# Kernel tuning notes

Hardware: AMD Instinct MI355X
Metric: run time of the kernel (lower is better)

## Reference

```python
import jax, jax.numpy as jnp
import numpy as np

ENZ_DIM, CPD_DIM, OUT_DIM = 1280, 256, 512
B, L_ENZ, L_CPD = 32, 512, 128
SCALE = OUT_DIM ** 0.5


def _linear_params(key, d_in, d_out):
    k1, k2 = jax.random.split(key)
    lim = 1.0 / np.sqrt(d_in)
    W = jax.random.uniform(k1, (d_in, d_out), jnp.float32, -lim, lim)
    b = jax.random.uniform(k2, (d_out,), jnp.float32, -lim, lim)
    return W, b


def setup_inputs() -> dict:
    key = jax.random.key(0)
    ks = jax.random.split(key, 16)
    inp = {
        "enz_node_feature": jax.random.normal(ks[0], (B, L_ENZ, ENZ_DIM), jnp.float32),
        "substrate_node_feature": jax.random.normal(ks[1], (B, L_CPD, CPD_DIM), jnp.float32),
        "product_node_feature": jax.random.normal(ks[2], (B, L_CPD, CPD_DIM), jnp.float32),
        "enz_node_feature_mask": jnp.ones((B, L_ENZ), dtype=bool),
        "substrate_node_feature_mask": jnp.ones((B, L_CPD), dtype=bool),
        "product_node_feature_mask": jnp.ones((B, L_CPD), dtype=bool),
        "interaction_weight": jax.random.normal(ks[3], (B, L_CPD, L_ENZ), jnp.float32),
    }
    # cross_attn_enzyme: query=enz (ENZ_DIM), key/value=cpd (CPD_DIM)
    inp["enz_Wq"], inp["enz_bq"] = _linear_params(ks[4], ENZ_DIM, OUT_DIM)
    inp["enz_Wk"], inp["enz_bk"] = _linear_params(ks[5], CPD_DIM, OUT_DIM)
    inp["enz_Wv"], inp["enz_bv"] = _linear_params(ks[6], CPD_DIM, OUT_DIM)
    # cross_attn_substrate: query=cpd, key/value=enz
    inp["sub_Wq"], inp["sub_bq"] = _linear_params(ks[7], CPD_DIM, OUT_DIM)
    inp["sub_Wk"], inp["sub_bk"] = _linear_params(ks[8], ENZ_DIM, OUT_DIM)
    inp["sub_Wv"], inp["sub_bv"] = _linear_params(ks[9], ENZ_DIM, OUT_DIM)
    # cross_attn_product: query=cpd, key/value=enz
    inp["prod_Wq"], inp["prod_bq"] = _linear_params(ks[10], CPD_DIM, OUT_DIM)
    inp["prod_Wk"], inp["prod_bk"] = _linear_params(ks[11], ENZ_DIM, OUT_DIM)
    inp["prod_Wv"], inp["prod_bv"] = _linear_params(ks[12], ENZ_DIM, OUT_DIM)
    return inp


def _cross_attn(q_in, k_in, v_in, q_mask, k_mask, Wq, bq, Wk, bk, Wv, bv, attn_bias=None):
    q = q_in @ Wq + bq          # [B, Lq, D]
    k = k_in @ Wk + bk          # [B, Lk, D]
    v = v_in @ Wv + bv          # [B, Lk, D]
    scores = jnp.einsum("bqd,bkd->bqk", q, k) / SCALE
    if attn_bias is not None:
        scores = scores + attn_bias
    mask = q_mask[:, :, None] & k_mask[:, None, :]   # [B, Lq, Lk]
    scores = jnp.where(mask, scores, -1e9)
    w = jax.nn.softmax(scores, axis=-1)
    return jnp.einsum("bqk,bkd->bqd", w, v)


def reference(enz_node_feature, substrate_node_feature, product_node_feature,
              enz_node_feature_mask, substrate_node_feature_mask, product_node_feature_mask,
              interaction_weight,
              enz_Wq, enz_bq, enz_Wk, enz_bk, enz_Wv, enz_bv,
              sub_Wq, sub_bq, sub_Wk, sub_bk, sub_Wv, sub_bv,
              prod_Wq, prod_bq, prod_Wk, prod_bk, prod_Wv, prod_bv):
    subs_pocket_weight = interaction_weight                       # [B, L_cpd, L_enz]
    pocket_subs_weight = jnp.swapaxes(interaction_weight, 1, 2)   # [B, L_enz, L_cpd]

    enzyme_subs = _cross_attn(enz_node_feature, substrate_node_feature, substrate_node_feature,
                              enz_node_feature_mask, substrate_node_feature_mask,
                              enz_Wq, enz_bq, enz_Wk, enz_bk, enz_Wv, enz_bv,
                              attn_bias=pocket_subs_weight)
    subs_enzyme = _cross_attn(substrate_node_feature, enz_node_feature, enz_node_feature,
                              substrate_node_feature_mask, enz_node_feature_mask,
                              sub_Wq, sub_bq, sub_Wk, sub_bk, sub_Wv, sub_bv,
                              attn_bias=subs_pocket_weight)
    # product path reuses cross_attn_enzyme weights for enz->prod (as in torch code)
    enzyme_prod = _cross_attn(enz_node_feature, product_node_feature, product_node_feature,
                              enz_node_feature_mask, product_node_feature_mask,
                              enz_Wq, enz_bq, enz_Wk, enz_bk, enz_Wv, enz_bv)
    prod_enzyme = _cross_attn(product_node_feature, enz_node_feature, enz_node_feature,
                              product_node_feature_mask, enz_node_feature_mask,
                              prod_Wq, prod_bq, prod_Wk, prod_bk, prod_Wv, prod_bv)

    return jnp.concatenate([enzyme_subs.mean(axis=1), subs_enzyme.mean(axis=1),
                            enzyme_prod.mean(axis=1), prod_enzyme.mean(axis=1)], axis=-1)
```

## Files before the change

kernel.cpp:

```cpp
#include <hip/hip_runtime.h>
#include <cstdint>
#include <cstddef>


#define SCALE_INV 0.044194173824159216f

typedef short bf16x8 __attribute__((ext_vector_type(8)));
typedef float f32x4  __attribute__((ext_vector_type(4)));

__device__ __forceinline__ ushort f2bf(float f) {
  union { float f; unsigned u; } c; c.f = f;
  unsigned u = c.u + 0x7fffu + ((c.u >> 16) & 1u);
  return (ushort)(u >> 16);
}
__device__ __forceinline__ float bf2f(ushort h) {
  return __uint_as_float(((unsigned)h) << 16);
}
__device__ __forceinline__ void gload16(const ushort* g, ushort* l) {
  __builtin_amdgcn_global_load_lds(
      (const __attribute__((address_space(1))) void*)g,
      (__attribute__((address_space(3))) void*)l, 16, 0, 0);
}

__device__ __forceinline__ void cvt8(const float* __restrict__ in,
                                     ushort* __restrict__ out, int blk, int n) {
  int i = (blk * 256 + (int)threadIdx.x) * 8;
  if (i >= n) return;
  float4 a = *(const float4*)(in + i);
  float4 b = *(const float4*)(in + i + 4);
  ushort o[8] = { f2bf(a.x), f2bf(a.y), f2bf(a.z), f2bf(a.w),
                  f2bf(b.x), f2bf(b.y), f2bf(b.z), f2bf(b.w) };
  *(uint4*)(out + i) = *(uint4*)o;
}

__global__ __launch_bounds__(256) void prep_fused(
    const float* __restrict__ enz, const float* __restrict__ sub,
    const float* __restrict__ prod,
    ushort* __restrict__ enz_b, ushort* __restrict__ sub_b, ushort* __restrict__ prod_b,
    const float* __restrict__ enz_Wq, const float* __restrict__ enz_Wk,
    const float* __restrict__ sub_Wq, const float* __restrict__ sub_Wk,
    const float* __restrict__ prod_Wq, const float* __restrict__ prod_Wk,
    ushort* __restrict__ eWq_b, ushort* __restrict__ eWk_b,
    ushort* __restrict__ sWq_b, ushort* __restrict__ sWk_b,
    ushort* __restrict__ pWq_b, ushort* __restrict__ pWk_b,
    const float* __restrict__ enz_bq, const float* __restrict__ sub_bq,
    const float* __restrict__ prod_bq,
    const float* __restrict__ enz_bv, const float* __restrict__ sub_bv,
    const float* __restrict__ prod_bv,
    float* __restrict__ u_s_s, float* __restrict__ u_p_s,
    float* __restrict__ u_e_s,
    float* __restrict__ zero_base, float* __restrict__ out)
{
  const int f = blockIdx.x, t = threadIdx.x;
  if (f < 10240) { cvt8(enz, enz_b, f, 20971520); return; }
  if (f < 10752) { cvt8(sub, sub_b, f - 10240, 1048576); return; }
  if (f < 11264) { cvt8(prod, prod_b, f - 10752, 1048576); return; }
  if (f < 12416) {
    const int l = f - 11264;
    if (l < 320)       cvt8(enz_Wq,  eWq_b, l,        655360);
    else if (l < 640)  cvt8(sub_Wk,  sWk_b, l - 320,  655360);
    else if (l < 960)  cvt8(prod_Wk, pWk_b, l - 640,  655360);
    else if (l < 1024) cvt8(enz_Wk,  eWk_b, l - 960,  131072);
    else if (l < 1088) cvt8(sub_Wq,  sWq_b, l - 1024, 131072);
    else               cvt8(prod_Wq, pWq_b, l - 1088, 131072);
    return;
  }
  if (f < 12592) {
    const int g = f - 12416;
    const float* W; const float* bv; float* U; int d0;
    if (g < 80)       { W = sub_Wk;  bv = sub_bq;  U = u_s_s; d0 = g * 16; }
    else if (g < 160) { W = prod_Wk; bv = prod_bq; U = u_p_s; d0 = (g - 80) * 16; }
    else              { W = enz_Wk;  bv = enz_bq;  U = u_e_s; d0 = (g - 160) * 16; }
    const int r = t >> 4, i = t & 15, d = d0 + r;
    const float* row = W + (size_t)d * 512;
    float s = 0.f;
#pragma unroll
    for (int j = 0; j < 32; j++) s += row[i + j * 16] * bv[i + j * 16];
    s += __shfl_xor(s, 1); s += __shfl_xor(s, 2);
    s += __shfl_xor(s, 4); s += __shfl_xor(s, 8);
    if (i == 0) U[d] = s * SCALE_INV;
    return;
  }
  if (f < 13168) { zero_base[(f - 12592) * 256 + t] = 0.f; return; }
  {
    const int idx = (f - 13168) * 256 + t;
    const int col = idx & 2047;
    const int q = col >> 9, n = col & 511;
    const float* bvp = (q == 1) ? sub_bv : (q == 3) ? prod_bv : enz_bv;
    out[idx] = bvp[n];
  }
}

__device__ __forceinline__ void mfma_tile(
    const ushort* __restrict__ A, int lda,
    const ushort* __restrict__ Bt, int ldb, int K,
    int bm, int bn, ushort* AsBase, ushort* BsBase, f32x4 (&acc)[4][4])
{
  const int t = threadIdx.x, wave = t >> 6, lane = t & 63;
  const int srow = wave * 16 + (lane >> 2);
  const int sseg = (lane & 3) * 8;
  const ushort* Ag0 = A + (size_t)(bm + srow) * lda + sseg;
  const ushort* Ag1 = Ag0 + (size_t)64 * lda;
  const ushort* Bg0 = Bt + (size_t)(bn + srow) * ldb + sseg;
  const ushort* Bg1 = Bg0 + (size_t)64 * ldb;
  ushort* AsP0 = AsBase + srow * 32 + sseg;
  ushort* AsP1 = AsP0 + 64 * 32;
  ushort* BsP0 = BsBase + srow * 32 + sseg;
  ushort* BsP1 = BsP0 + 64 * 32;
  const int wm = (wave >> 1) * 64, wn = (wave & 1) * 64;
  const int fl = lane & 15, fq = lane >> 4;
  const bf16x8* ArP = (const bf16x8*)(AsBase + (wm + fl) * 32 + fq * 8);
  const bf16x8* BrP = (const bf16x8*)(BsBase + (wn + fl) * 32 + fq * 8);
  for (int k0 = 0; k0 < K; k0 += 32) {
    __syncthreads();
    gload16(Ag0 + k0, AsP0);
    gload16(Ag1 + k0, AsP1);
    gload16(Bg0 + k0, BsP0);
    gload16(Bg1 + k0, BsP1);
    __syncthreads();
    bf16x8 af[4], bfr[4];
#pragma unroll
    for (int i = 0; i < 4; i++) af[i] = ArP[i * 64];
#pragma unroll
    for (int j = 0; j < 4; j++) bfr[j] = BrP[j * 64];
#pragma unroll
    for (int i = 0; i < 4; i++)
#pragma unroll
      for (int j = 0; j < 4; j++)
        acc[i][j] = __builtin_amdgcn_mfma_f32_16x16x32_bf16(af[i], bfr[j], acc[i][j], 0, 0, 0);
  }
}

__global__ __launch_bounds__(256) void fold_w3(
    const ushort* __restrict__ eWq_b, const ushort* __restrict__ eWk_b,
    const ushort* __restrict__ sWq_b, const ushort* __restrict__ sWk_b,
    const ushort* __restrict__ pWq_b, const ushort* __restrict__ pWk_b,
    const ushort* __restrict__ sub_b, const ushort* __restrict__ prod_b,
    const ushort* __restrict__ enz_b,
    const float* __restrict__ u_e_s, const float* __restrict__ u_s_s,
    const float* __restrict__ u_p_s,
    ushort* __restrict__ W3t, float* __restrict__ t_es, float* __restrict__ t_ep,
    float* __restrict__ t_se, float* __restrict__ t_pe)
{
  __shared__ __align__(16) ushort As[128 * 32];
  __shared__ __align__(16) ushort Bs[128 * 32];
  __shared__ float us[256];
  __shared__ float us2[2][1280];
  const int f = blockIdx.x, t = threadIdx.x;
  if (f >= 76) {
    const int g2 = f - 76;
    for (int i = t; i < 1280; i += 256) { us2[0][i] = u_s_s[i]; us2[1][i] = u_p_s[i]; }
    __syncthreads();
    const int row = g2 * 64 + (t >> 2), lane4 = t & 3;
    const ushort* xr = enz_b + (size_t)row * 1280;
    float ss = 0.f, sp = 0.f;
#pragma unroll
    for (int q = 0; q < 40; ++q) {
      const int c0 = q * 32 + lane4 * 8;
      bf16x8 v = *(const bf16x8*)(xr + c0);
#pragma unroll
      for (int i = 0; i < 8; ++i) {
        const float x = bf2f((ushort)v[i]);
        ss += x * us2[0][c0 + i];
        sp += x * us2[1][c0 + i];
      }
    }
    ss += __shfl_xor(ss, 1); ss += __shfl_xor(ss, 2);
    sp += __shfl_xor(sp, 1); sp += __shfl_xor(sp, 2);
    if (lane4 == 0) { t_se[row] = ss; t_pe[row] = sp; }
    return;
  }
  if (f >= 60) {
    const int g = f - 60, path = g >> 3, blk8 = g & 7;
    const ushort* Xb = path ? prod_b : sub_b;
    float* T = path ? t_ep : t_es;
    us[t] = u_e_s[t];
    __syncthreads();
#pragma unroll
    for (int e = 0; e < 2; ++e) {
      const int row = blk8 * 512 + e * 256 + t;
      const ushort* xr = Xb + (size_t)row * 256;
      float s = 0.f;
      for (int c = 0; c < 256; c += 8) {
        bf16x8 v = *(const bf16x8*)(xr + c);
#pragma unroll
        for (int i = 0; i < 8; ++i) s += bf2f((ushort)v[i]) * us[c + i];
      }
      T[row] = s;
    }
    return;
  }
  const int seg = f / 20, l = f % 20;
  const int bm = (l / 10) * 128, bn = (l % 10) * 128;
  const ushort* A  = (seg == 0) ? eWk_b : (seg == 1) ? sWq_b : pWq_b;
  const ushort* Bt = (seg == 0) ? eWq_b : (seg == 1) ? sWk_b : pWk_b;
  f32x4 acc[4][4] = {};
  mfma_tile(A, 512, Bt, 512, 512, bm, bn, As, Bs, acc);
  const int lane = t & 63, wave = t >> 6;
  const int wm = (wave >> 1) * 64, wn = (wave & 1) * 64;
  const int fl = lane & 15, fq = lane >> 4;
#pragma unroll
  for (int i = 0; i < 4; i++)
#pragma unroll
    for (int j = 0; j < 4; j++) {
      const int col = bn + wn + j * 16 + fl;
#pragma unroll
      for (int r = 0; r < 4; r++) {
        const int row = seg * 256 + bm + wm + i * 16 + fq * 4 + r;
        W3t[(size_t)row * 1280 + col] = f2bf(acc[i][j][r]);
      }
    }
}

__device__ __forceinline__ void yg_stage_unit(
    const ushort* __restrict__ gbase, int k0, int u,
    ushort* ldsTile, int wv, int l, int srow8, int scol)
{
  const int row0 = u * 64 + wv * 8 + srow8;
  gload16(gbase + (size_t)row0 * 1280 + k0 + scol,
          ldsTile + u * 4096 + wv * 512 + l * 8);
}

__device__ __forceinline__ bf16x8 yg_frag(const ushort* tile, int row, int kk, int fq) {
  const int X = (kk * 64 + fq * 16) ^ ((row & 7) << 4);
  return *(const bf16x8*)((const char*)tile + row * 128 + X);
}

__global__ __launch_bounds__(512, 4) void y_gemm(
    const ushort* __restrict__ A,
    const ushort* __restrict__ B,
    ushort* __restrict__ Y)
{
  extern __shared__ __align__(16) ushort lds[];
  const int t = threadIdx.x;
  const int wv = t >> 6, l = t & 63;
  const int fl = l & 15, fq = l >> 4;
  const int f = blockIdx.x;
  const int xcd = f & 7, slot = f >> 3;
  const int mt = xcd * 16 + (slot >> 2), nt = slot & 3;
  const int bm = mt * 128, bn = nt * 192;
  const int wm = (wv >> 2) * 64, wn = (wv & 3) * 48;
  const int srow8 = l >> 3;
  const int scol = 8 * ((l & 7) ^ srow8);
  const ushort* Ag = A + (size_t)bm * 1280;
  const ushort* Bg = B + (size_t)bn * 1280;

  ushort* A0 = lds;
  ushort* B0 = lds + 8192;
  ushort* A1 = lds + 20480;
  ushort* B1 = lds + 28672;

  f32x4 acc[4][3] = {};

#pragma unroll
  for (int u = 0; u < 2; ++u) yg_stage_unit(Ag, 0, u, A0, wv, l, srow8, scol);
#pragma unroll
  for (int u = 0; u < 3; ++u) yg_stage_unit(Bg, 0, u, B0, wv, l, srow8, scol);
#pragma unroll
  for (int u = 0; u < 2; ++u) yg_stage_unit(Ag, 64, u, A1, wv, l, srow8, scol);
  asm volatile("s_waitcnt vmcnt(2)" ::: "memory");
  __builtin_amdgcn_s_barrier();
  __builtin_amdgcn_sched_barrier(0);

  for (int j = 0; j < 20; ++j) {
    const int p = j & 1;
    const ushort* At = p ? A1 : A0;
    const ushort* Bt = p ? B1 : B0;
    ushort* Bo = p ? B0 : B1;
    const int kn = (j + 1) * 64;

    bf16x8 bf_[3][2];
#pragma unroll
    for (int n = 0; n < 3; ++n)
#pragma unroll
      for (int kk = 0; kk < 2; ++kk)
        bf_[n][kk] = yg_frag(Bt, wn + n * 16 + fl, kk, fq);

#pragma unroll
    for (int mp = 0; mp < 4; ++mp) {
      if (mp < 3 && j < 19) yg_stage_unit(Bg, kn, mp, Bo, wv, l, srow8, scol);
      bf16x8 a0[2];
#pragma unroll
      for (int kk = 0; kk < 2; ++kk)
        a0[kk] = yg_frag(At, wm + mp * 16 + fl, kk, fq);
      __builtin_amdgcn_s_setprio(1);
#pragma unroll
      for (int kk = 0; kk < 2; ++kk)
#pragma unroll
        for (int n = 0; n < 3; ++n)
          acc[mp][n] = __builtin_amdgcn_mfma_f32_16x16x32_bf16(
              a0[kk], bf_[n][kk], acc[mp][n], 0, 0, 0);
      __builtin_amdgcn_s_setprio(0);
    }

    asm volatile("" ::: "memory");
    __builtin_amdgcn_s_barrier();
    if (j + 2 < 20) {
      ushort* Ao = (ushort*)At;
#pragma unroll
      for (int u = 0; u < 2; ++u)
        yg_stage_unit(Ag, (j + 2) * 64, u, Ao, wv, l, srow8, scol);
    }
    if (j < 18) asm volatile("s_waitcnt vmcnt(2)" ::: "memory");
    else        asm volatile("s_waitcnt vmcnt(0)" ::: "memory");
    __builtin_amdgcn_s_barrier();
    __builtin_amdgcn_sched_barrier(0);
  }

#pragma unroll
  for (int m = 0; m < 4; ++m)
#pragma unroll
    for (int n = 0; n < 3; ++n)
#pragma unroll
      for (int r = 0; r < 4; ++r) {
        const int row = bm + wm + m * 16 + fq * 4 + r;
        const int col = bn + wn + n * 16 + fl;
        Y[(size_t)row * 768 + col] = f2bf(acc[m][n][r]);
      }
}

__global__ __launch_bounds__(256) void score_fused(
    const ushort* __restrict__ Y, const ushort* __restrict__ sub_b,
    const ushort* __restrict__ prod_b, const float* __restrict__ iw,
    const float* __restrict__ t_es, const float* __restrict__ t_ep,
    const float* __restrict__ t_se, const float* __restrict__ t_pe,
    float* __restrict__ Sc_se, float* __restrict__ Sc_pe,
    float* __restrict__ l_se, float* __restrict__ l_pe,
    float* __restrict__ wsum_es, float* __restrict__ wsum_ep)
{
  __shared__ __align__(16) ushort As[128 * 32];
  __shared__ __align__(16) ushort Bs[128 * 32];
  __shared__ float red[2][128];
  __shared__ float red2[2][128];
  const int f = blockIdx.x, t = threadIdx.x;
  const int lane = t & 63, wave = t >> 6;
  const int wm = (wave >> 1) * 64, wn = (wave & 1) * 64;
  const int fl = lane & 15, fq = lane >> 4;
  f32x4 acc[4][4] = {};

  if (f < 256) {
    const int path = f >> 7, l = f & 127, b = l & 31, mt = l >> 5;
    const int bm = mt * 128;
    const ushort* X = (path ? prod_b : sub_b) + (size_t)b * 32768;
    mfma_tile(Y + (size_t)b * 512 * 768, 768, X, 256, 256, bm, 0, As, Bs, acc);
    const size_t ib = (size_t)b * 65536;
    const float* Tp = (path ? t_ep : t_es) + b * 128;
    float tvv[4];
#pragma unroll
    for (int j = 0; j < 4; j++) tvv[j] = Tp[wn + j * 16 + fl];
    float rsum[4][4];
#pragma unroll
    for (int i = 0; i < 4; i++)
#pragma unroll
      for (int r = 0; r < 4; r++) rsum[i][r] = 0.f;
#pragma unroll
    for (int i = 0; i < 4; i++)
#pragma unroll
      for (int j = 0; j < 4; j++)
#pragma unroll
        for (int r = 0; r < 4; r++) {
          const int row = wm + i * 16 + fq * 4 + r;
          const int col = wn + j * 16 + fl;
          float s = acc[i][j][r] * SCALE_INV + tvv[j];
          if (path == 0) s += iw[ib + (size_t)col * 512 + (bm + row)];
          const float e = __expf(s);
          acc[i][j][r] = e;
          rsum[i][r] += e;
        }
#pragma unroll
    for (int m = 1; m <= 8; m <<= 1)
#pragma unroll
      for (int i = 0; i < 4; i++)
#pragma unroll
        for (int r = 0; r < 4; r++)
          rsum[i][r] += __shfl_xor(rsum[i][r], m);
    if (fl == 0)
#pragma unroll
      for (int i = 0; i < 4; i++)
#pragma unroll
        for (int r = 0; r < 4; r++)
          red[wave & 1][wm + i * 16 + fq * 4 + r] = rsum[i][r];
    __syncthreads();
    float csum[4] = { 0.f, 0.f, 0.f, 0.f };
#pragma unroll
    for (int i = 0; i < 4; i++)
#pragma unroll
      for (int r = 0; r < 4; r++) {
        const int row = wm + i * 16 + fq * 4 + r;
        const float invr = 1.f / (red[0][row] + red[1][row]);
#pragma unroll
        for (int j = 0; j < 4; j++) csum[j] += acc[i][j][r] * invr;
      }
#pragma unroll
    for (int m = 16; m <= 32; m <<= 1)
#pragma unroll
      for (int j = 0; j < 4; j++) csum[j] += __shfl_xor(csum[j], m);
    if (fq == 0)
#pragma unroll
      for (int j = 0; j < 4; j++) red2[wave >> 1][wn + j * 16 + fl] = csum[j];
    __syncthreads();
    float* ws = (path ? wsum_ep : wsum_es) + b * 128;
    if (t < 128) atomicAdd(&ws[t], red2[0][t] + red2[1][t]);
  } else {
    const int g = f - 256, path = g >> 7, l = g & 127, b = l & 31, nt = l >> 5;
    const int bn = nt * 128;
    const ushort* A  = (path ? prod_b : sub_b) + (size_t)b * 32768;
    const ushort* Bt = Y + (size_t)b * 512 * 768 + 256 + path * 256;
    mfma_tile(A, 256, Bt, 768, 256, 0, bn, As, Bs, acc);
    const size_t ib = (size_t)b * 65536;
    float* Sc = (path ? Sc_pe : Sc_se) + ib;
    const float* Tq = (path ? t_pe : t_se) + b * 512;
    float tv[4];
#pragma unroll
    for (int j = 0; j < 4; j++) tv[j] = Tq[bn + wn + j * 16 + fl];
    float rsum[4][4];
#pragma unroll
    for (int i = 0; i < 4; i++)
#pragma unroll
      for (int r = 0; r < 4; r++) rsum[i][r] = 0.f;
#pragma unroll
    for (int i = 0; i < 4; i++)
#pragma unroll
      for (int j = 0; j < 4; j++)
#pragma unroll
        for (int r = 0; r < 4; r++) {
          const int row = wm + i * 16 + fq * 4 + r;
          const int col = wn + j * 16 + fl;
          float s = acc[i][j][r] * SCALE_INV + tv[j];
          if (path == 0) s += iw[ib + (size_t)row * 512 + (bn + col)];
          const float e = __expf(s);
          Sc[(size_t)row * 512 + bn + col] = e;
          rsum[i][r] += e;
        }
#pragma unroll
    for (int m = 1; m <= 8; m <<= 1)
#pragma unroll
      for (int i = 0; i < 4; i++)
#pragma unroll
        for (int r = 0; r < 4; r++)
          rsum[i][r] += __shfl_xor(rsum[i][r], m);
    if (fl == 0)
#pragma unroll
      for (int i = 0; i < 4; i++)
#pragma unroll
        for (int r = 0; r < 4; r++)
          red[wave & 1][wm + i * 16 + fq * 4 + r] = rsum[i][r];
    __syncthreads();
    float* lr = (path ? l_pe : l_se) + b * 128;
    if (t < 128) atomicAdd(&lr[t], red[0][t] + red[1][t]);
  }
}

__global__ __launch_bounds__(256) void colsum2(
    const float* __restrict__ Sc_se, const float* __restrict__ Sc_pe,
    const float* __restrict__ l_se, const float* __restrict__ l_pe,
    float* __restrict__ wsum_se, float* __restrict__ wsum_pe)
{
  __shared__ float inv[32];
  const int f = blockIdx.x, t = threadIdx.x;
  const int path = f >> 7, l = f & 127, b = l & 31, qc = l >> 5;
  const float* Sc = (path ? Sc_pe : Sc_se) + (size_t)b * 65536 + (size_t)(qc * 32) * 512;
  const float* lv = (path ? l_pe : l_se) + b * 128 + qc * 32;
  float* ws = (path ? wsum_pe : wsum_se) + b * 512;
  if (t < 32) inv[t] = 1.f / lv[t];
  __syncthreads();
  float a0 = 0.f, a1 = 0.f;
  for (int q = 0; q < 32; q++) {
    const float iq = inv[q];
    a0 += Sc[(size_t)q * 512 + t] * iq;
    a1 += Sc[(size_t)q * 512 + 256 + t] * iq;
  }
  atomicAdd(&ws[t], a0);
  atomicAdd(&ws[t + 256], a1);
}

__global__ __launch_bounds__(256) void wx_fused(
    const float* __restrict__ wsum_se, const float* __restrict__ wsum_pe,
    const float* __restrict__ wsum_es, const float* __restrict__ wsum_ep,
    const ushort* __restrict__ enz_b, const ushort* __restrict__ sub_b,
    const ushort* __restrict__ prod_b,
    float* __restrict__ wx_se, float* __restrict__ wx_pe,
    float* __restrict__ wx_es, float* __restrict__ wx_ep)
{
  __shared__ float wse[256], wpe[256];
  const int f = blockIdx.x, t = threadIdx.x;
  if (f < 320) {
    const int ch = f % 5, tmp = f / 5, b = tmp & 31, kh = tmp >> 5;
    wse[t] = wsum_se[b * 512 + kh * 256 + t];
    wpe[t] = wsum_pe[b * 512 + kh * 256 + t];
    __syncthreads();
    const int c = ch * 256 + t;
    const ushort* X = enz_b + (size_t)b * 512 * 1280 + (size_t)(kh * 256) * 1280 + c;
    float a_se = 0.f, a_pe = 0.f;
#pragma unroll 4
    for (int k = 0; k < 256; k++) {
      const float x = bf2f(X[(size_t)k * 1280]);
      a_se += wse[k] * x;
      a_pe += wpe[k] * x;
    }
    atomicAdd(&wx_se[b * 1280 + c], a_se);
    atomicAdd(&wx_pe[b * 1280 + c], a_pe);
  } else if (f < 352) {
    const int b = f - 320;
    const ushort* X = sub_b + (size_t)b * 128 * 256 + t;
    float a = 0.f;
#pragma unroll 4
    for (int k = 0; k < 128; k++) a += wsum_es[b * 128 + k] * bf2f(X[(size_t)k * 256]);
    wx_es[b * 256 + t] = a;
  } else {
    const int b = f - 352;
    const ushort* X = prod_b + (size_t)b * 128 * 256 + t;
    float a = 0.f;
#pragma unroll 4
    for (int k = 0; k < 128; k++) a += wsum_ep[b * 128 + k] * bf2f(X[(size_t)k * 256]);
    wx_ep[b * 256 + t] = a;
  }
}

__global__ __launch_bounds__(256) void out_gemv(
    const float* __restrict__ wx_es, const float* __restrict__ wx_se,
    const float* __restrict__ wx_ep, const float* __restrict__ wx_pe,
    const float* __restrict__ enz_Wv, const float* __restrict__ sub_Wv,
    const float* __restrict__ prod_Wv,
    float* __restrict__ out)
{
  __shared__ float sw[32][64];
  const int f = blockIdx.x, t = threadIdx.x;
  const float* wx; const float* Wv; int Cdim, qoff, nb, cc; float inv;
  if (f < 40)      { wx = wx_se; Wv = sub_Wv;  Cdim = 1280; inv = 1.f / 128.f; qoff = 512;  nb = f & 1;        cc = f >> 1; }
  else if (f < 80) { wx = wx_pe; Wv = prod_Wv; Cdim = 1280; inv = 1.f / 128.f; qoff = 1536; nb = (f - 40) & 1; cc = (f - 40) >> 1; }
  else if (f < 88) { wx = wx_es; Wv = enz_Wv;  Cdim = 256;  inv = 1.f / 512.f; qoff = 0;    nb = (f - 80) & 1; cc = (f - 80) >> 1; }
  else             { wx = wx_ep; Wv = enz_Wv;  Cdim = 256;  inv = 1.f / 512.f; qoff = 1024; nb = (f - 88) & 1; cc = (f - 88) >> 1; }
  const int c0 = cc * 64, n = nb * 256 + t;
#pragma unroll
  for (int i = 0; i < 8; i++) {
    const int idx = t + i * 256, b = idx >> 6, c = idx & 63;
    sw[b][c] = wx[(size_t)b * Cdim + c0 + c];
  }
  __syncthreads();
  float acc[32];
#pragma unroll
  for (int b = 0; b < 32; b++) acc[b] = 0.f;
  for (int c = 0; c < 64; c += 4) {
    const float w0 = Wv[(size_t)(c0 + c) * 512 + n];
    const float w1 = Wv[(size_t)(c0 + c + 1) * 512 + n];
    const float w2 = Wv[(size_t)(c0 + c + 2) * 512 + n];
    const float w3 = Wv[(size_t)(c0 + c + 3) * 512 + n];
#pragma unroll
    for (int b = 0; b < 32; b++) {
      const float4 s = *(const float4*)&sw[b][c];
      acc[b] += s.x * w0 + s.y * w1 + s.z * w2 + s.w * w3;
    }
  }
#pragma unroll
  for (int b = 0; b < 32; b++)
    atomicAdd(&out[(size_t)b * 2048 + qoff + n], acc[b] * inv);
}

extern "C" void kernel_launch(void* const* d_in, const int* in_sizes, int n_in,
                              void* d_out, int out_size, void* d_ws, size_t ws_size,
                              hipStream_t stream)
{
  (void)in_sizes; (void)n_in; (void)out_size; (void)ws_size;
  const float* enz     = (const float*)d_in[0];
  const float* sub     = (const float*)d_in[1];
  const float* prod    = (const float*)d_in[2];
  const float* iw      = (const float*)d_in[6];
  const float* enz_Wq  = (const float*)d_in[7];
  const float* enz_bq  = (const float*)d_in[8];
  const float* enz_Wk  = (const float*)d_in[9];
  const float* enz_Wv  = (const float*)d_in[11];
  const float* enz_bv  = (const float*)d_in[12];
  const float* sub_Wq  = (const float*)d_in[13];
  const float* sub_bq  = (const float*)d_in[14];
  const float* sub_Wk  = (const float*)d_in[15];
  const float* sub_Wv  = (const float*)d_in[17];
  const float* sub_bv  = (const float*)d_in[18];
  const float* prod_Wq = (const float*)d_in[19];
  const float* prod_bq = (const float*)d_in[20];
  const float* prod_Wk = (const float*)d_in[21];
  const float* prod_Wv = (const float*)d_in[23];
  const float* prod_bv = (const float*)d_in[24];
  float* out = (float*)d_out;

  char* wsb = (char*)d_ws;
  size_t off = 0;
  auto alloc = [&](size_t bytes) {
    void* p = wsb + off;
    off += (bytes + 255) & ~(size_t)255;
    return p;
  };
  ushort* enz_b   = (ushort*)alloc((size_t)32 * 512 * 1280 * 2);
  ushort* sub_b   = (ushort*)alloc((size_t)32 * 128 * 256 * 2);
  ushort* prod_b  = (ushort*)alloc((size_t)32 * 128 * 256 * 2);
  ushort* eWq_b   = (ushort*)alloc((size_t)1280 * 512 * 2);
  ushort* sWk_b   = (ushort*)alloc((size_t)1280 * 512 * 2);
  ushort* pWk_b   = (ushort*)alloc((size_t)1280 * 512 * 2);
  ushort* eWk_b   = (ushort*)alloc((size_t)256 * 512 * 2);
  ushort* sWq_b   = (ushort*)alloc((size_t)256 * 512 * 2);
  ushort* pWq_b   = (ushort*)alloc((size_t)256 * 512 * 2);
  ushort* W3t     = (ushort*)alloc((size_t)768 * 1280 * 2);
  ushort* Y       = (ushort*)alloc((size_t)16384 * 768 * 2);
  float*  u_s_s   = (float*)alloc(1280 * 4);
  float*  u_p_s   = (float*)alloc(1280 * 4);
  float*  u_e_s   = (float*)alloc(256 * 4);
  float*  t_es    = (float*)alloc(4096 * 4);
  float*  t_ep    = (float*)alloc(4096 * 4);
  float*  t_se    = (float*)alloc(16384 * 4);
  float*  t_pe    = (float*)alloc(16384 * 4);
  float*  Sc_se   = (float*)alloc((size_t)32 * 128 * 512 * 4);
  float*  Sc_pe   = (float*)alloc((size_t)32 * 128 * 512 * 4);
  float* wsum_es = (float*)alloc(4096 * 4);
  float* wsum_ep = (float*)alloc(4096 * 4);
  float* wsum_se = (float*)alloc(16384 * 4);
  float* wsum_pe = (float*)alloc(16384 * 4);
  float* l_se    = (float*)alloc(4096 * 4);
  float* l_pe    = (float*)alloc(4096 * 4);
  float* wx_se   = (float*)alloc(40960 * 4);
  float* wx_pe   = (float*)alloc(40960 * 4);
  float* wx_es   = (float*)alloc(8192 * 4);
  float* wx_ep   = (float*)alloc(8192 * 4);

  static bool ygemm_attr_set = false;
  if (!ygemm_attr_set) {
    hipFuncSetAttribute(reinterpret_cast<const void*>(y_gemm),
                        hipFuncAttributeMaxDynamicSharedMemorySize, 81920);
    ygemm_attr_set = true;
  }

  const dim3 blk(256);

  prep_fused<<<13424, blk, 0, stream>>>(
      enz, sub, prod, enz_b, sub_b, prod_b,
      enz_Wq, enz_Wk, sub_Wq, sub_Wk, prod_Wq, prod_Wk,
      eWq_b, eWk_b, sWq_b, sWk_b, pWq_b, pWk_b,
      enz_bq, sub_bq, prod_bq, enz_bv, sub_bv, prod_bv,
      u_s_s, u_p_s, u_e_s, wsum_es, out);

  fold_w3<<<332, blk, 0, stream>>>(
      eWq_b, eWk_b, sWq_b, sWk_b, pWq_b, pWk_b,
      sub_b, prod_b, enz_b, u_e_s, u_s_s, u_p_s,
      W3t, t_es, t_ep, t_se, t_pe);

  y_gemm<<<512, 512, 81920, stream>>>(enz_b, W3t, Y);

  score_fused<<<512, blk, 0, stream>>>(
      Y, sub_b, prod_b, iw, t_es, t_ep, t_se, t_pe,
      Sc_se, Sc_pe, l_se, l_pe, wsum_es, wsum_ep);

  colsum2<<<256, blk, 0, stream>>>(Sc_se, Sc_pe, l_se, l_pe, wsum_se, wsum_pe);

  wx_fused<<<384, blk, 0, stream>>>(
      wsum_se, wsum_pe, wsum_es, wsum_ep, enz_b, sub_b, prod_b,
      wx_se, wx_pe, wx_es, wx_ep);

  out_gemv<<<96, blk, 0, stream>>>(
      wx_es, wx_se, wx_ep, wx_pe, enz_Wv, sub_Wv, prod_Wv, out);
}
```

Baseline: 314.9 us.

## Use K=64 XOR-swizzled LDS tiles in MFMA GEMM and transpose score tile

Replaces the K=32 MFMA tile loop with a K=64 variant that stages A/B tiles with an XOR swizzle on 16-byte segments. This halves the number of barrier pairs per K and is meant to avoid LDS bank conflicts on fragment reads. The first score path now computes the transposed product (cpd rows by enzyme columns), so interaction_weight reads run along contiguous rows. The softmax and column-sum reductions are reordered to match the new orientation. LDS per block doubles, which may reduce occupancy.

```diff
diff --git a/kernel.cpp b/kernel.cpp
--- a/kernel.cpp
+++ b/kernel.cpp
@@ -91,43 +91,46 @@
   }
 }
 
-__device__ __forceinline__ void mfma_tile(
+__device__ __forceinline__ void mfma_tile64(
     const ushort* __restrict__ A, int lda,
     const ushort* __restrict__ Bt, int ldb, int K,
     int bm, int bn, ushort* AsBase, ushort* BsBase, f32x4 (&acc)[4][4])
 {
   const int t = threadIdx.x, wave = t >> 6, lane = t & 63;
-  const int srow = wave * 16 + (lane >> 2);
-  const int sseg = (lane & 3) * 8;
-  const ushort* Ag0 = A + (size_t)(bm + srow) * lda + sseg;
-  const ushort* Ag1 = Ag0 + (size_t)64 * lda;
-  const ushort* Bg0 = Bt + (size_t)(bn + srow) * ldb + sseg;
-  const ushort* Bg1 = Bg0 + (size_t)64 * ldb;
-  ushort* AsP0 = AsBase + srow * 32 + sseg;
-  ushort* AsP1 = AsP0 + 64 * 32;
-  ushort* BsP0 = BsBase + srow * 32 + sseg;
-  ushort* BsP1 = BsP0 + 64 * 32;
+  const int r8 = lane >> 3;
+  const int csrc = 8 * ((lane & 7) ^ r8);
   const int wm = (wave >> 1) * 64, wn = (wave & 1) * 64;
   const int fl = lane & 15, fq = lane >> 4;
-  const bf16x8* ArP = (const bf16x8*)(AsBase + (wm + fl) * 32 + fq * 8);
-  const bf16x8* BrP = (const bf16x8*)(BsBase + (wn + fl) * 32 + fq * 8);
-  for (int k0 = 0; k0 < K; k0 += 32) {
-    __syncthreads();
-    gload16(Ag0 + k0, AsP0);
-    gload16(Ag1 + k0, AsP1);
-    gload16(Bg0 + k0, BsP0);
-    gload16(Bg1 + k0, BsP1);
-    __syncthreads();
-    bf16x8 af[4], bfr[4];
-#pragma unroll
-    for (int i = 0; i < 4; i++) af[i] = ArP[i * 64];
-#pragma unroll
-    for (int j = 0; j < 4; j++) bfr[j] = BrP[j * 64];
-#pragma unroll
-    for (int i = 0; i < 4; i++)
-#pragma unroll
-      for (int j = 0; j < 4; j++)
-        acc[i][j] = __builtin_amdgcn_mfma_f32_16x16x32_bf16(af[i], bfr[j], acc[i][j], 0, 0, 0);
+  for (int k0 = 0; k0 < K; k0 += 64) {
+    __syncthreads();
+#pragma unroll
+    for (int i = 0; i < 4; i++) {
+      const int row = i * 32 + wave * 8 + r8;
+      ushort* dst = AsBase + row * 64 + (lane & 7) * 8;
+      gload16(A + (size_t)(bm + row) * lda + k0 + csrc, dst);
+      gload16(Bt + (size_t)(bn + row) * ldb + k0 + csrc,
+              BsBase + row * 64 + (lane & 7) * 8);
+    }
+    __syncthreads();
+#pragma unroll
+    for (int kk = 0; kk < 2; kk++) {
+      bf16x8 bfr[4];
+#pragma unroll
+      for (int j = 0; j < 4; j++) {
+        const int row = wn + j * 16 + fl;
+        bfr[j] = *(const bf16x8*)(BsBase + row * 64 +
+                                  8 * (((kk << 2) + fq) ^ (row & 7)));
+      }
+#pragma unroll
+      for (int i = 0; i < 4; i++) {
+        const int row = wm + i * 16 + fl;
+        bf16x8 af = *(const bf16x8*)(AsBase + row * 64 +
+                                     8 * (((kk << 2) + fq) ^ (row & 7)));
+#pragma unroll
+        for (int j = 0; j < 4; j++)
+          acc[i][j] = __builtin_amdgcn_mfma_f32_16x16x32_bf16(af, bfr[j], acc[i][j], 0, 0, 0);
+      }
+    }
   }
 }
 
@@ -142,8 +145,8 @@
     ushort* __restrict__ W3t, float* __restrict__ t_es, float* __restrict__ t_ep,
     float* __restrict__ t_se, float* __restrict__ t_pe)
 {
-  __shared__ __align__(16) ushort As[128 * 32];
-  __shared__ __align__(16) ushort Bs[128 * 32];
+  __shared__ __align__(16) ushort As[128 * 64];
+  __shared__ __align__(16) ushort Bs[128 * 64];
   __shared__ float us[256];
   __shared__ float us2[2][1280];
   const int f = blockIdx.x, t = threadIdx.x;
@@ -195,7 +198,7 @@
   const ushort* A  = (seg == 0) ? eWk_b : (seg == 1) ? sWq_b : pWq_b;
   const ushort* Bt = (seg == 0) ? eWq_b : (seg == 1) ? sWk_b : pWk_b;
   f32x4 acc[4][4] = {};
-  mfma_tile(A, 512, Bt, 512, 512, bm, bn, As, Bs, acc);
+  mfma_tile64(A, 512, Bt, 512, 512, bm, bn, As, Bs, acc);
   const int lane = t & 63, wave = t >> 6;
   const int wm = (wave >> 1) * 64, wn = (wave & 1) * 64;
   const int fl = lane & 15, fq = lane >> 4;
@@ -328,8 +331,8 @@
     float* __restrict__ l_se, float* __restrict__ l_pe,
     float* __restrict__ wsum_es, float* __restrict__ wsum_ep)
 {
-  __shared__ __align__(16) ushort As[128 * 32];
-  __shared__ __align__(16) ushort Bs[128 * 32];
+  __shared__ __align__(16) ushort As[128 * 64];
+  __shared__ __align__(16) ushort Bs[128 * 64];
   __shared__ float red[2][128];
   __shared__ float red2[2][128];
   const int f = blockIdx.x, t = threadIdx.x;
@@ -339,20 +342,19 @@
   f32x4 acc[4][4] = {};
 
   if (f < 256) {
-    const int path = f >> 7, l = f & 127, b = l & 31, mt = l >> 5;
-    const int bm = mt * 128;
-    const ushort* X = (path ? prod_b : sub_b) + (size_t)b * 32768;
-    mfma_tile(Y + (size_t)b * 512 * 768, 768, X, 256, 256, bm, 0, As, Bs, acc);
+    const int path = f >> 7, l = f & 127, b = l & 31, qt = l >> 5;
+    const int bn = qt * 128;
+    const ushort* X  = (path ? prod_b : sub_b) + (size_t)b * 32768;
+    const ushort* Yb = Y + (size_t)b * 512 * 768;
+    mfma_tile64(X, 256, Yb, 768, 256, 0, bn, As, Bs, acc);
     const size_t ib = (size_t)b * 65536;
     const float* Tp = (path ? t_ep : t_es) + b * 128;
-    float tvv[4];
-#pragma unroll
-    for (int j = 0; j < 4; j++) tvv[j] = Tp[wn + j * 16 + fl];
-    float rsum[4][4];
+    float tvv[4][4];
 #pragma unroll
     for (int i = 0; i < 4; i++)
 #pragma unroll
-      for (int r = 0; r < 4; r++) rsum[i][r] = 0.f;
+      for (int r = 0; r < 4; r++) tvv[i][r] = Tp[wm + i * 16 + fq * 4 + r];
+    float csum[4] = { 0.f, 0.f, 0.f, 0.f };
 #pragma unroll
     for (int i = 0; i < 4; i++)
 #pragma unroll
@@ -361,12 +363,37 @@
         for (int r = 0; r < 4; r++) {
           const int row = wm + i * 16 + fq * 4 + r;
           const int col = wn + j * 16 + fl;
-          float s = acc[i][j][r] * SCALE_INV + tvv[j];
-          if (path == 0) s += iw[ib + (size_t)col * 512 + (bm + row)];
+          float s = acc[i][j][r] * SCALE_INV + tvv[i][r];
+          if (path == 0) s += iw[ib + (size_t)row * 512 + (bn + col)];
           const float e = __expf(s);
           acc[i][j][r] = e;
-          rsum[i][r] += e;
+          csum[j] += e;
         }
+#pragma unroll
+    for (int m = 16; m <= 32; m <<= 1)
+#pragma unroll
+      for (int j = 0; j < 4; j++) csum[j] += __shfl_xor(csum[j], m);
+    if (fq == 0)
+#pragma unroll
+      for (int j = 0; j < 4; j++) red[wave >> 1][wn + j * 16 + fl] = csum[j];
+    __syncthreads();
+    float invc[4];
+#pragma unroll
+    for (int j = 0; j < 4; j++) {
+      const int col = wn + j * 16 + fl;
+      invc[j] = 1.f / (red[0][col] + red[1][col]);
+    }
+    float rsum[4][4];
+#pragma unroll
+    for (int i = 0; i < 4; i++)
+#pragma unroll
+      for (int r = 0; r < 4; r++) rsum[i][r] = 0.f;
+#pragma unroll
+    for (int i = 0; i < 4; i++)
+#pragma unroll
+      for (int j = 0; j < 4; j++)
+#pragma unroll
+        for (int r = 0; r < 4; r++) rsum[i][r] += acc[i][j][r] * invc[j];
 #pragma unroll
     for (int m = 1; m <= 8; m <<= 1)
 #pragma unroll
@@ -379,25 +406,7 @@
       for (int i = 0; i < 4; i++)
 #pragma unroll
         for (int r = 0; r < 4; r++)
-          red[wave & 1][wm + i * 16 + fq * 4 + r] = rsum[i][r];
-    __syncthreads();
-    float csum[4] = { 0.f, 0.f, 0.f, 0.f };
-#pragma unroll
-    for (int i = 0; i < 4; i++)
-#pragma unroll
-      for (int r = 0; r < 4; r++) {
-        const int row = wm + i * 16 + fq * 4 + r;
-        const float invr = 1.f / (red[0][row] + red[1][row]);
-#pragma unroll
-        for (int j = 0; j < 4; j++) csum[j] += acc[i][j][r] * invr;
-      }
-#pragma unroll
-    for (int m = 16; m <= 32; m <<= 1)
-#pragma unroll
-      for (int j = 0; j < 4; j++) csum[j] += __shfl_xor(csum[j], m);
-    if (fq == 0)
-#pragma unroll
-      for (int j = 0; j < 4; j++) red2[wave >> 1][wn + j * 16 + fl] = csum[j];
+          red2[wave & 1][wm + i * 16 + fq * 4 + r] = rsum[i][r];
     __syncthreads();
     float* ws = (path ? wsum_ep : wsum_es) + b * 128;
     if (t < 128) atomicAdd(&ws[t], red2[0][t] + red2[1][t]);
@@ -406,7 +415,7 @@
     const int bn = nt * 128;
     const ushort* A  = (path ? prod_b : sub_b) + (size_t)b * 32768;
     const ushort* Bt = Y + (size_t)b * 512 * 768 + 256 + path * 256;
-    mfma_tile(A, 256, Bt, 768, 256, 0, bn, As, Bs, acc);
+    mfma_tile64(A, 256, Bt, 768, 256, 0, bn, As, Bs, acc);
     const size_t ib = (size_t)b * 65536;
     float* Sc = (path ? Sc_pe : Sc_se) + ib;
     const float* Tq = (path ? t_pe : t_se) + b * 512;
```

New measurement: 314.9 us. About the same (+0.0%).
